# Kernel optimization log

Measured on AMD Instinct MI355X. Metric: run time of the kernel, lower is better.

The kernel has to match this reference:

```python
import jax, jax.numpy as jnp
import numpy as np

B, S, C, E, F, K = 4, 2048, 1024, 8, 2752, 2


def setup_inputs() -> dict:
    key = jax.random.key(0)
    k0, k1, k2, k3, k4 = jax.random.split(key, 5)
    std = 0.02
    return {
        "x": jax.random.normal(k0, (B, S, C), dtype=jnp.float32),
        "w_gate": jax.random.normal(k1, (E, C), dtype=jnp.float32) * std,
        "wg": jax.random.normal(k2, (E, C, F), dtype=jnp.float32) * std,
        "wu": jax.random.normal(k3, (E, C, F), dtype=jnp.float32) * std,
        "wd": jax.random.normal(k4, (E, F, C), dtype=jnp.float32) * std,
        "k": K,
    }


def reference(x, w_gate, wg, wu, wd, k):
    b, s, c = x.shape
    n_experts = w_gate.shape[0]
    # Gate: softmax over experts, top-k, normalized weights (norm_topk_prob=True)
    logits = jnp.einsum('bsc,ec->bse', x, w_gate)
    scores = jax.nn.softmax(logits, axis=-1)
    topk_w, topk_i = jax.lax.top_k(scores, k)            # [b,s,k]
    topk_w = topk_w / (topk_w.sum(axis=-1, keepdims=True) + 1e-9)

    t = b * s
    x_flat = x.reshape(t, c)
    # Dense combine matrix [T, E]: weight of expert e for token t (0 if not routed)
    combine = jnp.zeros((t, n_experts), dtype=x.dtype)
    combine = combine.at[jnp.arange(t)[:, None], topk_i.reshape(t, k)].add(topk_w.reshape(t, k))

    # Per-expert SwiGLU MLP, weighted combine (loop over fixed small E)
    out = jnp.zeros_like(x_flat)
    for e in range(n_experts):
        h = jax.nn.silu(x_flat @ wg[e]) * (x_flat @ wu[e])   # [T, F]
        out = out + combine[:, e:e + 1] * (h @ wd[e])         # [T, C]
    return out.reshape(b, s, c)
```

## Files before the change

kernel.cpp:

```cpp
#include <hip/hip_runtime.h>

#define Tn      8192
#define Cn      1024
#define En      8
#define Fn      2752
#define MAXROWS 18432
#define NT1     32
#define NT2     86

typedef __bf16 bf16;
typedef bf16  bf16x8 __attribute__((ext_vector_type(8)));
typedef bf16  bf16x4 __attribute__((ext_vector_type(4)));
typedef float f32x4  __attribute__((ext_vector_type(4)));

__device__ __forceinline__ void gload16(const bf16* g, bf16* l) {
  __builtin_amdgcn_global_load_lds(
      (const __attribute__((address_space(1))) unsigned int*)g,
      (__attribute__((address_space(3))) unsigned int*)l, 16, 0, 0);
}

#define BARRIER() __builtin_amdgcn_s_barrier()
#define VMCNT(N)  asm volatile("s_waitcnt vmcnt(" #N ")" ::: "memory")
#define MFMA(d, va, vb) d = __builtin_amdgcn_mfma_f32_16x16x32_bf16(va, vb, d, 0, 0, 0)

__device__ __forceinline__ int xcd_swz(int flat, int nwg) {
  int xcd = flat & 7, loc = flat >> 3;
  int q = nwg >> 3, r = nwg & 7;
  return (xcd < r ? xcd * (q + 1) : r * (q + 1) + (xcd - r) * q) + loc;
}

__global__ __launch_bounds__(256) void prep_kernel(
    const float* __restrict__ wg, const float* __restrict__ wu,
    bf16* __restrict__ guT,
    const float* __restrict__ x, const float* __restrict__ wgate,
    int* __restrict__ topk_i, float* __restrict__ topk_w,
    bf16* __restrict__ xgd)
{
  const int id = blockIdx.x;
  if (id >= 11008) {
    int lane = threadIdx.x & 63;
    int wid  = threadIdx.x >> 6;
    int t = (id - 11008) * 4 + wid;
    const float4* xr4 = (const float4*)(x + (size_t)t * Cn);
    bf16* xo = xgd + (size_t)t * Cn;
    float acc[En];
#pragma unroll
    for (int e = 0; e < En; ++e) acc[e] = 0.f;
#pragma unroll
    for (int i = 0; i < 4; ++i) {
      int c4 = i * 64 + lane;
      float4 xv = xr4[c4];
      bf16x4 pv;
      pv[0] = (bf16)xv.x; pv[1] = (bf16)xv.y; pv[2] = (bf16)xv.z; pv[3] = (bf16)xv.w;
      *(bf16x4*)(xo + c4 * 4) = pv;
#pragma unroll
      for (int e = 0; e < En; ++e) {
        const float4 wv = *(const float4*)(wgate + e * Cn + c4 * 4);
        acc[e] = fmaf(xv.x, wv.x, acc[e]);
        acc[e] = fmaf(xv.y, wv.y, acc[e]);
        acc[e] = fmaf(xv.z, wv.z, acc[e]);
        acc[e] = fmaf(xv.w, wv.w, acc[e]);
      }
    }
#pragma unroll
    for (int e = 0; e < En; ++e) {
#pragma unroll
      for (int o = 32; o > 0; o >>= 1) acc[e] += __shfl_xor(acc[e], o, 64);
    }
    if (lane == 0) {
      float mx = acc[0];
#pragma unroll
      for (int e = 1; e < En; ++e) mx = fmaxf(mx, acc[e]);
      float p[En], Z = 0.f;
#pragma unroll
      for (int e = 0; e < En; ++e) { p[e] = __expf(acc[e] - mx); Z += p[e]; }
      int i0 = 0;
#pragma unroll
      for (int e = 1; e < En; ++e) if (p[e] > p[i0]) i0 = e;
      int i1 = (i0 == 0) ? 1 : 0;
#pragma unroll
      for (int e = 0; e < En; ++e) if (e != i0 && p[e] > p[i1]) i1 = e;
      float s0 = p[i0] / Z, s1 = p[i1] / Z;
      float inv = 1.f / (s0 + s1 + 1e-9f);
      topk_i[2 * t] = i0;       topk_i[2 * t + 1] = i1;
      topk_w[2 * t] = s0 * inv; topk_w[2 * t + 1] = s1 * inv;
    }
    return;
  }
  int z = id / 688, rem = id % 688;
  const int bm = (rem % 16) * 64;
  const int bn = (rem / 16) * 64;
  const float* src = (z < En ? wg : wu) + (size_t)(z & 7) * Cn * Fn;
  bf16* dst = guT + (size_t)z * Cn * Fn;
  const int M = Cn, N = Fn;

  __shared__ float L[64][65];
  const int tid = threadIdx.x;
  const int mr = tid >> 4, nseg = tid & 15;
#pragma unroll
  for (int p = 0; p < 4; ++p) {
    int m = p * 16 + mr;
    float4 v = *(const float4*)(src + (size_t)(bm + m) * N + bn + nseg * 4);
    L[nseg * 4 + 0][m] = v.x;
    L[nseg * 4 + 1][m] = v.y;
    L[nseg * 4 + 2][m] = v.z;
    L[nseg * 4 + 3][m] = v.w;
  }
  __syncthreads();
  const int nr = tid >> 3, mseg = tid & 7;
#pragma unroll
  for (int q = 0; q < 2; ++q) {
    int n = q * 32 + nr;
    bf16x8 w;
#pragma unroll
    for (int j = 0; j < 8; ++j) w[j] = (bf16)L[n][mseg * 8 + j];
    *(bf16x8*)(dst + (size_t)(bn + n) * M + bm + mseg * 8) = w;
  }
}

__global__ __launch_bounds__(256) void offsets_kernel(
    const int* __restrict__ topk_i, int* __restrict__ counts,
    int* __restrict__ fill, int* __restrict__ off, int* __restrict__ tok_list)
{
  __shared__ int lc[4][En];
  __shared__ int offl[En + 1];
  __shared__ int cntl[En];
  const int tid = threadIdx.x;
  const int w = tid >> 6;
  if (tid < 4 * En) lc[tid >> 3][tid & 7] = 0;
  __syncthreads();
  for (int i = tid; i < Tn * 2; i += 256)
    atomicAdd(&lc[w][topk_i[i]], 1);
  __syncthreads();
  if (tid == 0) {
    int o = 0;
    for (int e = 0; e < En; ++e) {
      int c = lc[0][e] + lc[1][e] + lc[2][e] + lc[3][e];
      cntl[e] = c;
      counts[e] = c;
      off[e]  = o;
      fill[e] = o;
      offl[e] = o;
      o += (c + 255) & ~255;
    }
    off[En] = o;
    offl[En] = o;
  }
  __syncthreads();
  for (int e = 0; e < En; ++e) {
    int lo = offl[e] + cntl[e], hi = offl[e + 1];
    for (int r = lo + tid; r < hi; r += 256) tok_list[r] = -1;
  }
}

__global__ __launch_bounds__(256) void scatter_kernel(
    const int* __restrict__ topk_i, const float* __restrict__ topk_w,
    int* __restrict__ fill, int* __restrict__ tok_list, float* __restrict__ wgt_list,
    int* __restrict__ inv_rows)
{
  __shared__ int lc[En];
  __shared__ int base[En];
  const int tid = threadIdx.x;
  const int t = blockIdx.x * 256 + tid;
  if (tid < En) lc[tid] = 0;
  __syncthreads();
  int e0 = topk_i[2 * t], e1 = topk_i[2 * t + 1];
  int r0 = atomicAdd(&lc[e0], 1);
  int r1 = atomicAdd(&lc[e1], 1);
  __syncthreads();
  if (tid < En) base[tid] = atomicAdd(&fill[tid], lc[tid]);
  __syncthreads();
  int p0 = base[e0] + r0, p1 = base[e1] + r1;
  tok_list[p0] = t; wgt_list[p0] = topk_w[2 * t];     inv_rows[2 * t]     = p0;
  tok_list[p1] = t; wgt_list[p1] = topk_w[2 * t + 1]; inv_rows[2 * t + 1] = p1;
}


__global__ __launch_bounds__(256, 2) void gemm1_kernel(
    const bf16* __restrict__ xgd, const int* __restrict__ tok_list,
    const bf16* __restrict__ wgT, const bf16* __restrict__ wuT,
    const int* __restrict__ off, const int* __restrict__ counts,
    const float* __restrict__ wgt_list, bf16* __restrict__ h, int row_lo,
    const float* __restrict__ wd, bf16* __restrict__ wdT, int ngemm)
{
  __shared__ bf16 sm[3][12288];

  const int flat = blockIdx.x;
  const int tid = threadIdx.x;

  if (flat >= ngemm) {
    int id2 = flat - ngemm;
    int z = id2 / 688, rem = id2 % 688;
    const int bm = (rem % 43) * 64;
    const int bn = (rem / 43) * 64;
    const float* src = wd + (size_t)z * Fn * Cn;
    bf16* dst = wdT + (size_t)z * Fn * Cn;
    const int M = Fn, N = Cn;
    float (*L)[65] = reinterpret_cast<float(*)[65]>(&sm[0][0]);

    const int mr = tid >> 4, nseg = tid & 15;
#pragma unroll
    for (int p = 0; p < 4; ++p) {
      int m = p * 16 + mr;
      float4 v = *(const float4*)(src + (size_t)(bm + m) * N + bn + nseg * 4);
      L[nseg * 4 + 0][m] = v.x;
      L[nseg * 4 + 1][m] = v.y;
      L[nseg * 4 + 2][m] = v.z;
      L[nseg * 4 + 3][m] = v.w;
    }
    __syncthreads();
    const int nr = tid >> 3, mseg = tid & 7;
#pragma unroll
    for (int q = 0; q < 2; ++q) {
      int n = q * 32 + nr;
      bf16x8 w;
#pragma unroll
      for (int j = 0; j < 8; ++j) w[j] = (bf16)L[n][mseg * 8 + j];
      *(bf16x8*)(dst + (size_t)(bn + n) * M + bm + mseg * 8) = w;
    }
    return;
  }

  const int gdx = 43;
  const int gdy = ngemm / 43;
  const int s = xcd_swz(flat, ngemm);
  int bx, by;
  if ((gdy & 7) == 0) {
    const int gsz = gdx * 8;
    int grp = s / gsz, rem = s % gsz;
    bx = rem >> 3;
    by = grp * 8 + (rem & 7);
  } else { bx = s % gdx; by = s / gdx; }

  const int m0 = row_lo + by * 256;
  if (m0 >= off[En]) return;
  int e = 0;
  while (off[e + 1] <= m0) ++e;
  const int base = off[e], cnt = counts[e];
  const int n0 = bx * 64;

  const int lane = tid & 63, wid = tid >> 6;
  const int wm  = (wid & 1) * 128;
  const int wnv = (wid >> 1) * 32;
  const int fr = lane & 15, q = lane >> 4;
  const int lrow = tid >> 2;
  const int gseg = (tid & 3) ^ ((tid >> 3) & 3);
  const int tt = (q ^ ((fr >> 1) & 3)) * 8;

  const bf16* wge = wgT + (size_t)e * ((size_t)Fn * Cn);
  const bf16* wue = wuT + (size_t)e * ((size_t)Fn * Cn);
  int tk0 = tok_list[m0 + lrow];        if (tk0 < 0) tk0 = 0;
  int tk1 = tok_list[m0 + 64 + lrow];   if (tk1 < 0) tk1 = 0;
  int tk2 = tok_list[m0 + 128 + lrow];  if (tk2 < 0) tk2 = 0;
  int tk3 = tok_list[m0 + 192 + lrow];  if (tk3 < 0) tk3 = 0;
  const bf16* ag0 = xgd + (size_t)tk0 * Cn + gseg * 8;
  const bf16* ag1 = xgd + (size_t)tk1 * Cn + gseg * 8;
  const bf16* ag2 = xgd + (size_t)tk2 * Cn + gseg * 8;
  const bf16* ag3 = xgd + (size_t)tk3 * Cn + gseg * 8;
  const bf16* bgp = wge + (size_t)(n0 + lrow) * Cn + gseg * 8;
  const bf16* bup = wue + (size_t)(n0 + lrow) * Cn + gseg * 8;

  f32x4 accg[8][2], accu[8][2];
#pragma unroll
  for (int mi = 0; mi < 8; ++mi)
#pragma unroll
    for (int ni = 0; ni < 2; ++ni) { accg[mi][ni] = (f32x4)(0.f); accu[mi][ni] = (f32x4)(0.f); }

#define STG1(SRC, KOFF, DST, DOFF) gload16((SRC) + (KOFF), (DST) + (DOFF) + tid * 8)
#define ISSUE1(DST, KO) do { \
    STG1(ag0, KO, DST, 0);    STG1(ag1, KO, DST, 2048); \
    STG1(ag2, KO, DST, 4096); STG1(ag3, KO, DST, 6144); \
    STG1(bgp, KO, DST, 8192); STG1(bup, KO, DST, 10240); } while (0)

  ISSUE1(&sm[0][0], 0);
  ISSUE1(&sm[1][0], 32);
  VMCNT(6);
  BARRIER();

  const bf16* Sc = &sm[0][0];
  const bf16* Sn = &sm[1][0];
  bf16*       Sf = &sm[2][0];

  for (int kt = 0; kt < NT1; ++kt) {
    bf16x8 a[8], bg[2], bu[2];
#pragma unroll
    for (int mi = 0; mi < 8; ++mi)
      a[mi] = *(const bf16x8*)(Sc + (wm + mi * 16 + fr) * 32 + tt);
#pragma unroll
    for (int ni = 0; ni < 2; ++ni) {
      bg[ni] = *(const bf16x8*)(Sc + 8192 + (wnv + ni * 16 + fr) * 32 + tt);
      bu[ni] = *(const bf16x8*)(Sc + 10240 + (wnv + ni * 16 + fr) * 32 + tt);
    }
    if (kt + 2 < NT1) ISSUE1(Sf, (kt + 2) * 32);

    __builtin_amdgcn_s_setprio(1);
#pragma unroll
    for (int mi = 0; mi < 8; ++mi)
#pragma unroll
      for (int ni = 0; ni < 2; ++ni) {
        MFMA(accg[mi][ni], a[mi], bg[ni]);
        MFMA(accu[mi][ni], a[mi], bu[ni]);
      }
    __builtin_amdgcn_s_setprio(0);

    if (kt < NT1 - 2)       { VMCNT(6); BARRIER(); }
    else if (kt == NT1 - 2) { VMCNT(0); BARRIER(); }
    const bf16* t0 = Sc; Sc = Sn; Sn = Sf; Sf = (bf16*)t0;
  }
#undef ISSUE1
#undef STG1

  const int rq = (lane >> 4) * 4, cl = lane & 15;
#pragma unroll
  for (int mi = 0; mi < 8; ++mi) {
#pragma unroll
    for (int r = 0; r < 4; ++r) {
      int grow = m0 + wm + mi * 16 + rq + r;
      float w = (grow - base < cnt) ? wgt_list[grow] : 0.f;
      bf16* hr = h + (size_t)(grow - row_lo) * Fn + n0;
#pragma unroll
      for (int ni = 0; ni < 2; ++ni) {
        float g = accg[mi][ni][r], u = accu[mi][ni][r];
        hr[wnv + ni * 16 + cl] = (bf16)(w * u * (g / (1.f + __expf(-g))));
      }
    }
  }
}

__global__ __launch_bounds__(256, 4) void gemm2_kernel(
    const bf16* __restrict__ h, const bf16* __restrict__ wdT,
    const int* __restrict__ off, bf16* __restrict__ h2, int row_lo)
{
  const int gdy = gridDim.y;
  const int nwg = 8 * gdy;
  const int s = xcd_swz(blockIdx.y * 8 + blockIdx.x, nwg);
  int bn, bm;
  if ((gdy & 7) == 0) {
    int grp = s >> 6, rem = s & 63;
    bn = rem >> 3;
    bm = grp * 8 + (rem & 7);
  } else { bn = s & 7; bm = s >> 3; }

  const int m0 = row_lo + bm * 128;
  if (m0 >= off[En]) return;
  int e = 0;
  while (off[e + 1] <= m0) ++e;
  const int n0 = bn * 128;

  __shared__ bf16 sm[2][8192];

  const int tid = threadIdx.x;
  const int lane = tid & 63, wid = tid >> 6;
  const int wrow = (wid & 1) * 64;
  const int wcol = (wid >> 1) * 64;
  const int fr = lane & 15, q = lane >> 4;
  const int lrow = tid >> 2;
  const int gseg = (tid & 3) ^ ((tid >> 3) & 3);
  const int tt = (q ^ ((fr >> 1) & 3)) * 8;

  const bf16* ap0 = h   + (size_t)(m0 - row_lo + lrow) * Fn + gseg * 8;
  const bf16* ap1 = ap0 + (size_t)64 * Fn;
  const bf16* bp0 = wdT + (size_t)e * Cn * Fn + (size_t)(n0 + lrow) * Fn + gseg * 8;
  const bf16* bp1 = bp0 + (size_t)64 * Fn;

  f32x4 acc[4][4];
#pragma unroll
  for (int mi = 0; mi < 4; ++mi)
#pragma unroll
    for (int ni = 0; ni < 4; ++ni) acc[mi][ni] = (f32x4)(0.f);

  {
    bf16* N = &sm[0][0];
    gload16(ap0, N + tid * 8);
    gload16(ap1, N + 2048 + tid * 8);
    gload16(bp0, N + 4096 + tid * 8);
    gload16(bp1, N + 6144 + tid * 8);
  }
  VMCNT(0);
  BARRIER();

  for (int kt = 0; kt < NT2; ++kt) {
    const bf16* S = &sm[kt & 1][0];
    bf16* Nx = &sm[(kt + 1) & 1][0];
    const int ko = (kt + 1) * 32;

    if (kt + 1 < NT2) {
      gload16(ap0 + ko, Nx + tid * 8);
      gload16(ap1 + ko, Nx + 2048 + tid * 8);
      gload16(bp0 + ko, Nx + 4096 + tid * 8);
      gload16(bp1 + ko, Nx + 6144 + tid * 8);
    }

    bf16x8 a[4], b[4];
#pragma unroll
    for (int mi = 0; mi < 4; ++mi)
      a[mi] = *(const bf16x8*)(S + (wrow + mi * 16 + fr) * 32 + tt);
#pragma unroll
    for (int ni = 0; ni < 4; ++ni)
      b[ni] = *(const bf16x8*)(S + 4096 + (wcol + ni * 16 + fr) * 32 + tt);

    __builtin_amdgcn_s_setprio(1);
#pragma unroll
    for (int mi = 0; mi < 4; ++mi)
#pragma unroll
      for (int ni = 0; ni < 4; ++ni)
        MFMA(acc[mi][ni], a[mi], b[ni]);
    __builtin_amdgcn_s_setprio(0);

    VMCNT(0);
    BARRIER();
  }

  const int rq = (lane >> 4) * 4, cl = lane & 15;
#pragma unroll
  for (int mi = 0; mi < 4; ++mi) {
#pragma unroll
    for (int r = 0; r < 4; ++r) {
      int grow = m0 + wrow + mi * 16 + rq + r;
      bf16* orow = h2 + (size_t)grow * Cn + n0;
#pragma unroll
      for (int ni = 0; ni < 4; ++ni)
        orow[wcol + ni * 16 + cl] = (bf16)acc[mi][ni][r];
    }
  }
}

__global__ __launch_bounds__(256) void combine_kernel(
    const bf16* __restrict__ h2, const int* __restrict__ inv_rows,
    float* __restrict__ out)
{
  int t = blockIdx.x;
  int r0 = inv_rows[2 * t], r1 = inv_rows[2 * t + 1];
  int c = threadIdx.x * 4;
  bf16x4 a = *(const bf16x4*)(h2 + (size_t)r0 * Cn + c);
  bf16x4 b = *(const bf16x4*)(h2 + (size_t)r1 * Cn + c);
  float4 v;
  v.x = (float)a[0] + (float)b[0];
  v.y = (float)a[1] + (float)b[1];
  v.z = (float)a[2] + (float)b[2];
  v.w = (float)a[3] + (float)b[3];
  *(float4*)(out + (size_t)t * Cn + c) = v;
}

extern "C" void kernel_launch(void* const* d_in, const int* in_sizes, int n_in,
                              void* d_out, int out_size, void* d_ws, size_t ws_size,
                              hipStream_t stream)
{
  const float* x     = (const float*)d_in[0];
  const float* wgate = (const float*)d_in[1];
  const float* wg    = (const float*)d_in[2];
  const float* wu    = (const float*)d_in[3];
  const float* wd    = (const float*)d_in[4];

  char* ws = (char*)d_ws;
  int* counts = (int*)ws;
  int* fill   = counts + 8;
  int* off    = fill + 8;
  size_t o = 256;
  int*   topk_i   = (int*)(ws + o);   o += (size_t)Tn * 2 * 4;
  float* topk_w   = (float*)(ws + o); o += (size_t)Tn * 2 * 4;
  int*   tok_list = (int*)(ws + o);   o += (size_t)MAXROWS * 4;
  float* wgt_list = (float*)(ws + o); o += (size_t)MAXROWS * 4;
  int*   inv_rows = (int*)(ws + o);   o += (size_t)Tn * 2 * 4;
  o = (o + 255) & ~(size_t)255;
  const size_t WSZ = (size_t)En * Fn * Cn;
  bf16* wgT = (bf16*)(ws + o); o += WSZ * 2 * 2;
  bf16* wuT = wgT + WSZ;
  bf16* wdT = (bf16*)(ws + o); o += WSZ * 2;
  bf16* xgd = (bf16*)(ws + o); o += (size_t)Tn * Cn * 2;
  bf16* h2  = (bf16*)(ws + o); o += (size_t)MAXROWS * Cn * 2;
  bf16* h   = (bf16*)(ws + o);

  size_t havail = ws_size > o ? ws_size - o : 0;
  long crows = (long)(havail / ((size_t)Fn * 2));
  crows &= ~(long)255;
  if (crows > MAXROWS) crows = MAXROWS;
  if (crows < 256) crows = 256;
  const int chunk_rows = (int)crows;
  const int nch = (MAXROWS + chunk_rows - 1) / chunk_rows;

  prep_kernel<<<11008 + Tn / 4, 256, 0, stream>>>(
      wg, wu, wgT, x, wgate, topk_i, topk_w, xgd);

  offsets_kernel<<<1, 256, 0, stream>>>(topk_i, counts, fill, off, tok_list);
  scatter_kernel<<<Tn / 256, 256, 0, stream>>>(topk_i, topk_w, fill, tok_list, wgt_list, inv_rows);

  for (int c = 0; c < nch; ++c) {
    int row_lo = c * chunk_rows;
    const int ngemm = 43 * (chunk_rows / 256);
    const int nwd = (c == 0) ? 5504 : 0;
    gemm1_kernel<<<ngemm + nwd, 256, 0, stream>>>(
        xgd, tok_list, wgT, wuT, off, counts, wgt_list, h, row_lo, wd, wdT, ngemm);
    gemm2_kernel<<<dim3(8, chunk_rows / 128), 256, 0, stream>>>(
        h, wdT, off, h2, row_lo);
  }
  combine_kernel<<<Tn, 256, 0, stream>>>(h2, inv_rows, (float*)d_out);
}
```

Measured before the change: 469.8 us.

## Load gate/up weight fragments directly into registers instead of staging through LDS

In the first expert GEMM, the gate and up weight tiles are no longer staged through shared memory. Each lane now loads its MFMA B fragments straight from global memory into registers, one k-step ahead. The shared buffers hold only the gathered activation rows, which cuts LDS use per block from 72 KB to 48 KB and removes the B-side LDS reads. In exchange, the two waves that share a column slice fetch the same weights twice from global memory. The register prefetch is also only one step deep, so global latency may be exposed at every k-step.

After: 561.3 us. 1.19x slower.

```diff
diff --git a/kernel.cpp b/kernel.cpp
--- a/kernel.cpp
+++ b/kernel.cpp
@@ -183,7 +183,7 @@
     const float* __restrict__ wgt_list, bf16* __restrict__ h, int row_lo,
     const float* __restrict__ wd, bf16* __restrict__ wdT, int ngemm)
 {
-  __shared__ bf16 sm[3][12288];
+  __shared__ bf16 sm[3][8192];
 
   const int flat = blockIdx.x;
   const int tid = threadIdx.x;
@@ -257,8 +257,10 @@
   const bf16* ag1 = xgd + (size_t)tk1 * Cn + gseg * 8;
   const bf16* ag2 = xgd + (size_t)tk2 * Cn + gseg * 8;
   const bf16* ag3 = xgd + (size_t)tk3 * Cn + gseg * 8;
-  const bf16* bgp = wge + (size_t)(n0 + lrow) * Cn + gseg * 8;
-  const bf16* bup = wue + (size_t)(n0 + lrow) * Cn + gseg * 8;
+  const bf16* pbg0 = wge + (size_t)(n0 + wnv +  0 + fr) * Cn + q * 8;
+  const bf16* pbg1 = wge + (size_t)(n0 + wnv + 16 + fr) * Cn + q * 8;
+  const bf16* pbu0 = wue + (size_t)(n0 + wnv +  0 + fr) * Cn + q * 8;
+  const bf16* pbu1 = wue + (size_t)(n0 + wnv + 16 + fr) * Cn + q * 8;
 
   f32x4 accg[8][2], accu[8][2];
 #pragma unroll
@@ -267,14 +269,17 @@
     for (int ni = 0; ni < 2; ++ni) { accg[mi][ni] = (f32x4)(0.f); accu[mi][ni] = (f32x4)(0.f); }
 
 #define STG1(SRC, KOFF, DST, DOFF) gload16((SRC) + (KOFF), (DST) + (DOFF) + tid * 8)
-#define ISSUE1(DST, KO) do { \
+#define ISSUE_A(DST, KO) do { \
     STG1(ag0, KO, DST, 0);    STG1(ag1, KO, DST, 2048); \
-    STG1(ag2, KO, DST, 4096); STG1(ag3, KO, DST, 6144); \
-    STG1(bgp, KO, DST, 8192); STG1(bup, KO, DST, 10240); } while (0)
-
-  ISSUE1(&sm[0][0], 0);
-  ISSUE1(&sm[1][0], 32);
-  VMCNT(6);
+    STG1(ag2, KO, DST, 4096); STG1(ag3, KO, DST, 6144); } while (0)
+
+  bf16x8 bg0 = *(const bf16x8*)(pbg0);
+  bf16x8 bg1 = *(const bf16x8*)(pbg1);
+  bf16x8 bu0 = *(const bf16x8*)(pbu0);
+  bf16x8 bu1 = *(const bf16x8*)(pbu1);
+  ISSUE_A(&sm[0][0], 0);
+  ISSUE_A(&sm[1][0], 32);
+  VMCNT(4);
   BARRIER();
 
   const bf16* Sc = &sm[0][0];
@@ -282,32 +287,35 @@
   bf16*       Sf = &sm[2][0];
 
   for (int kt = 0; kt < NT1; ++kt) {
-    bf16x8 a[8], bg[2], bu[2];
+    bf16x8 a[8];
 #pragma unroll
     for (int mi = 0; mi < 8; ++mi)
       a[mi] = *(const bf16x8*)(Sc + (wm + mi * 16 + fr) * 32 + tt);
-#pragma unroll
-    for (int ni = 0; ni < 2; ++ni) {
-      bg[ni] = *(const bf16x8*)(Sc + 8192 + (wnv + ni * 16 + fr) * 32 + tt);
-      bu[ni] = *(const bf16x8*)(Sc + 10240 + (wnv + ni * 16 + fr) * 32 + tt);
-    }
-    if (kt + 2 < NT1) ISSUE1(Sf, (kt + 2) * 32);
 
     __builtin_amdgcn_s_setprio(1);
 #pragma unroll
-    for (int mi = 0; mi < 8; ++mi)
-#pragma unroll
-      for (int ni = 0; ni < 2; ++ni) {
-        MFMA(accg[mi][ni], a[mi], bg[ni]);
-        MFMA(accu[mi][ni], a[mi], bu[ni]);
-      }
+    for (int mi = 0; mi < 8; ++mi) {
+      MFMA(accg[mi][0], a[mi], bg0);
+      MFMA(accg[mi][1], a[mi], bg1);
+      MFMA(accu[mi][0], a[mi], bu0);
+      MFMA(accu[mi][1], a[mi], bu1);
+    }
     __builtin_amdgcn_s_setprio(0);
 
-    if (kt < NT1 - 2)       { VMCNT(6); BARRIER(); }
-    else if (kt == NT1 - 2) { VMCNT(0); BARRIER(); }
+    if (kt + 1 < NT1) {
+      const int ko = (kt + 1) * 32;
+      bg0 = *(const bf16x8*)(pbg0 + ko);
+      bg1 = *(const bf16x8*)(pbg1 + ko);
+      bu0 = *(const bf16x8*)(pbu0 + ko);
+      bu1 = *(const bf16x8*)(pbu1 + ko);
+    }
+    if (kt + 2 < NT1) ISSUE_A(Sf, (kt + 2) * 32);
+
+    if (kt + 2 < NT1)      { VMCNT(8); BARRIER(); }
+    else if (kt + 1 < NT1) { VMCNT(4); BARRIER(); }
     const bf16* t0 = Sc; Sc = Sn; Sn = Sf; Sf = (bf16*)t0;
   }
-#undef ISSUE1
+#undef ISSUE_A
 #undef STG1
 
   const int rq = (lane >> 4) * 4, cl = lane & 15;
```
